# Kernel tuning notes

Hardware: AMD Instinct MI355X
Metric: run time of the kernel (lower is better)

Reference implementation:

```python
import jax, jax.numpy as jnp
import numpy as np

B = 16; DEMO = 5; COND = 50; QOI = 50
L = DEMO * (COND + 2 * QOI)  # 750
D = 1024; H = 16; HD = D // H; NL = 6; DFF = 4096
IN_DIM = 5; OUT_DIM = 2; MAXPOS = max(COND, QOI)
NEG = -1e9


def _build_consts():
    # token types per demo segment: 0=cond, 1=qoi_kv, 2=qoi_k (query)
    types, demo, pos = [], [], []
    for d in range(DEMO):
        types += [0] * COND + [1] * QOI + [2] * QOI
        demo += [d] * (COND + 2 * QOI)
        pos += list(range(COND)) + list(range(QOI)) + list(range(QOI))
    t = np.array(types); g = np.array(demo); p = np.array(pos)
    ti, tj = t[:, None], t[None, :]
    gi, gj = g[:, None], g[None, :]
    eye = np.arange(L)[:, None] == np.arange(L)[None, :]
    prev = (gj < gi) & (tj < 2)                      # attend to cond/qoi_kv of earlier demos
    same = (gj == gi) & ((tj == 0) | ((ti == 1) & (tj == 1)) | ((ti == 2) & eye))
    mask = prev | same                               # True = allowed
    out_idx = np.where(t == 2)[0]                    # qoi_k positions -> outputs
    return mask, p, out_idx


def setup_inputs():
    key = jax.random.key(0)
    ks = jax.random.split(key, 10)
    mask, pos, out_idx = _build_consts()
    s = 0.02
    return {
        'sequence': jax.random.normal(ks[0], (B, L, IN_DIM), jnp.float32),
        'pre_W': jax.random.normal(ks[1], (IN_DIM, D), jnp.float32) * s,
        'pre_b': jnp.zeros((D,), jnp.float32),
        'pe_table': jax.random.normal(ks[2], (MAXPOS, D), jnp.float32) * s,
        'Wqkv': jax.random.normal(ks[3], (NL, D, 3 * D), jnp.float32) * s,
        'bqkv': jnp.zeros((NL, 3 * D), jnp.float32),
        'Wo': jax.random.normal(ks[4], (NL, D, D), jnp.float32) * s,
        'bo': jnp.zeros((NL, D), jnp.float32),
        'ln1_g': jnp.ones((NL, D), jnp.float32), 'ln1_b': jnp.zeros((NL, D), jnp.float32),
        'ln2_g': jnp.ones((NL, D), jnp.float32), 'ln2_b': jnp.zeros((NL, D), jnp.float32),
        'W1': jax.random.normal(ks[5], (NL, D, DFF), jnp.float32) * s,
        'b1': jnp.zeros((NL, DFF), jnp.float32),
        'W2': jax.random.normal(ks[6], (NL, DFF, D), jnp.float32) * s,
        'b2': jnp.zeros((NL, D), jnp.float32),
        'post_W': jax.random.normal(ks[7], (D, OUT_DIM), jnp.float32) * s,
        'post_b': jnp.zeros((OUT_DIM,), jnp.float32),
        'basic_mask': jnp.asarray(mask),
        'index_pos': jnp.asarray(pos, jnp.int32),
        'out_idx': jnp.asarray(out_idx, jnp.int32),
    }


def _ln(x, g, b):
    m = jnp.mean(x, axis=-1, keepdims=True)
    v = jnp.var(x, axis=-1, keepdims=True)
    return (x - m) * jax.lax.rsqrt(v + 1e-5) * g + b


def _encoder(x, bias, Wqkv, bqkv, Wo, bo, ln1_g, ln1_b, ln2_g, ln2_b, W1, b1, W2, b2):
    scale = 1.0 / np.sqrt(HD)
    for l in range(NL):
        qkv = x @ Wqkv[l] + bqkv[l]                          # [B,L,3D]
        q, k, v = jnp.split(qkv, 3, axis=-1)
        hd = lambda t: t.reshape(B, L, H, HD).transpose(0, 2, 1, 3)
        q, k, v = hd(q), hd(k), hd(v)
        sc = jnp.einsum('bhqd,bhkd->bhqk', q, k) * scale + bias
        a = jax.nn.softmax(sc, axis=-1)
        o = jnp.einsum('bhqk,bhkd->bhqd', a, v).transpose(0, 2, 1, 3).reshape(B, L, D)
        x = _ln(x + o @ Wo[l] + bo[l], ln1_g[l], ln1_b[l])   # post-LN (torch default)
        h = jax.nn.gelu(x @ W1[l] + b1[l], approximate=False)
        x = _ln(x + h @ W2[l] + b2[l], ln2_g[l], ln2_b[l])
    return x


def reference(sequence, pre_W, pre_b, pe_table, Wqkv, bqkv, Wo, bo,
              ln1_g, ln1_b, ln2_g, ln2_b, W1, b1, W2, b2,
              post_W, post_b, basic_mask, index_pos, out_idx):
    x = sequence @ pre_W + pre_b + pe_table[index_pos]       # pre-projection + learned PE
    bias = jnp.where(basic_mask, 0.0, NEG)[None, None, :, :]  # ~basic_mask -> -inf additive
    x = _encoder(x, bias, Wqkv, bqkv, Wo, bo, ln1_g, ln1_b, ln2_g, ln2_b, W1, b1, W2, b2)
    y = x @ post_W + post_b                                  # [B,L,OUT_DIM]
    y = y[:, out_idx, :]                                     # select qoi_k outputs
    return y.reshape(B, DEMO, QOI, OUT_DIM)
```

## Files before the change

kernel.cpp:

```cpp
#include <hip/hip_runtime.h>


#define Bz  16
#define Lz  750
#define Dz  1024
#define Hz  16
#define HDz 64
#define NLz 6
#define DFFz 4096
#define Mz  (Bz*Lz)
#define VSTRIDE 768
#define QKVPART ((size_t)Bz*Hz*Lz*HDz)

typedef unsigned short u16;
typedef unsigned int   u32;
typedef unsigned long long u64;
typedef __attribute__((ext_vector_type(8))) short bf8;
typedef __attribute__((ext_vector_type(4))) float f4;
typedef __attribute__((ext_vector_type(4))) unsigned short u16x4;

__device__ __forceinline__ u16 f2b(float f){
  u32 u = __builtin_bit_cast(u32, f);
  u += 0x7fffu + ((u >> 16) & 1u);
  return (u16)(u >> 16);
}
__device__ __forceinline__ u32 cvtpk(float a, float b){
  u32 r;
  asm("v_cvt_pk_bf16_f32 %0, %1, %2" : "=v"(r) : "v"(a), "v"(b));
  return r;
}
__device__ __forceinline__ void glds16(const void* g, void* l){
  __builtin_amdgcn_global_load_lds((const __attribute__((address_space(1))) void*)g,
                                   (__attribute__((address_space(3))) void*)l, 16, 0, 0);
}

__global__ __launch_bounds__(256) void k_mask(u64* __restrict__ mb){
  const int idx = blockIdx.x*256 + threadIdx.x;
  if (idx >= Lz*12) return;
  const int q = idx / 12, kt = idx - q*12;
  const int gq = q/150, rq = q - gq*150;
  const int tq = rq < 50 ? 0 : (rq < 100 ? 1 : 2);
  u64 m = 0;
  for (int j = 0; j < 64; j++){
    const int k = kt*64 + j;
    if (k >= Lz) break;
    const int gk = k/150, rk = k - gk*150;
    const int tk = rk < 50 ? 0 : (rk < 100 ? 1 : 2);
    const bool prev = (gk < gq) && (tk < 2);
    const bool same = (gk == gq) && ((tk == 0) || (tq == 1 && tk == 1) || (tq == 2 && k == q));
    if (prev || same) m |= (1ull << j);
  }
  mb[idx] = m;
}

__global__ __launch_bounds__(256) void k_embed(const float* __restrict__ seq,
    const float* __restrict__ preW, const float* __restrict__ preb,
    const float* __restrict__ pe, float* __restrict__ x, u16* __restrict__ xb){
  const int m = blockIdx.x, t = threadIdx.x;
  const int l = m % Lz;
  const int r = l % 150;
  const int p = r < 50 ? r : (r < 100 ? r - 50 : r - 100);
  const float s0 = seq[m*5+0], s1 = seq[m*5+1], s2 = seq[m*5+2],
              s3 = seq[m*5+3], s4 = seq[m*5+4];
  const int d = t*4;
  f4 acc = *(const f4*)&preb[d];
  acc += *(const f4*)&pe[p*Dz + d];
  acc += s0 * *(const f4*)&preW[0*Dz + d];
  acc += s1 * *(const f4*)&preW[1*Dz + d];
  acc += s2 * *(const f4*)&preW[2*Dz + d];
  acc += s3 * *(const f4*)&preW[3*Dz + d];
  acc += s4 * *(const f4*)&preW[4*Dz + d];
  *(f4*)&x[(size_t)m*Dz + d] = acc;
  u16x4 hv = { f2b(acc.x), f2b(acc.y), f2b(acc.z), f2b(acc.w) };
  *(u16x4*)&xb[(size_t)m*Dz + d] = hv;
}

__global__ __launch_bounds__(256) void k_transpose(const float* __restrict__ W,
    u16* __restrict__ Wt, int K, int ldw){
  __shared__ float tile[32][33];
  const int tx = threadIdx.x, ty = threadIdx.y;
  const int n0 = blockIdx.x*32, k0 = blockIdx.y*32;
  #pragma unroll
  for (int i = 0; i < 4; i++){
    const int k = ty + i*8;
    tile[k][tx] = W[(size_t)(k0+k)*ldw + n0+tx];
  }
  __syncthreads();
  #pragma unroll
  for (int i = 0; i < 4; i++){
    const int n = ty + i*8;
    Wt[(size_t)(n0+n)*K + k0+tx] = f2b(tile[tx][n]);
  }
}

template<int EPI>
__global__ __launch_bounds__(256, 2) void k_gemm(
    const u16* __restrict__ A, const u16* __restrict__ Bt,
    int M, int N, int K, int lda, int ldc, int col0,
    const float* __restrict__ bias,
    float* __restrict__ xres, u16* __restrict__ outb, u16* __restrict__ vtb){
  __shared__ u16 As[128*64];
  __shared__ u16 Bs[128*64];
  const int t = threadIdx.x;
  const int m0 = blockIdx.x*128, n0 = blockIdx.y*128;
  const int w = t >> 6, lane = t & 63;
  const int wm = (w >> 1)*64, wn = (w & 1)*64;
  const int cl = lane & 15, g4 = lane >> 4;
  f4 acc[4][4] = {};
  const int srow = t >> 3, scol = (t & 7)*8;
  const int lds_off = srow*64 + scol;
  for (int k0 = 0; k0 < K; k0 += 64){
    #pragma unroll
    for (int c = 0; c < 4; c++){
      int ra = m0 + c*32 + srow; ra = ra < M ? ra : M-1;
      glds16(A + (size_t)ra*lda + k0 + scol, &As[c*2048 + lds_off]);
      const int rb = n0 + c*32 + srow;
      glds16(Bt + (size_t)rb*K + k0 + scol, &Bs[c*2048 + lds_off]);
    }
    __syncthreads();
    #pragma unroll
    for (int kk = 0; kk < 2; kk++){
      const int ko = kk*32 + g4*8;
      bf8 af[4], bfr[4];
      #pragma unroll
      for (int i = 0; i < 4; i++) af[i]  = *(const bf8*)&As[(wm + i*16 + cl)*64 + ko];
      #pragma unroll
      for (int j = 0; j < 4; j++) bfr[j] = *(const bf8*)&Bs[(wn + j*16 + cl)*64 + ko];
      #pragma unroll
      for (int i = 0; i < 4; i++)
        #pragma unroll
        for (int j = 0; j < 4; j++)
          acc[i][j] = __builtin_amdgcn_mfma_f32_16x16x32_bf16(af[i], bfr[j], acc[i][j], 0, 0, 0);
    }
    __syncthreads();
  }
  const int rl = g4*4;
  #pragma unroll
  for (int i = 0; i < 4; i++){
    #pragma unroll
    for (int j = 0; j < 4; j++){
      const int gn = n0 + wn + j*16 + cl;
      const float bsv = bias ? bias[gn] : 0.f;
      if constexpr (EPI == 0){
        const int part = gn >> 10;
        const int hh = (gn >> 6) & 15;
        const int dd = gn & 63;
        const int gm0 = m0 + wm + i*16 + rl;
        if (part == 2){
          if (gm0 + 3 < M){
            const int b = gm0 / Lz, lr0 = gm0 - b*Lz;
            const float v0 = acc[i][j][0] + bsv, v1 = acc[i][j][1] + bsv;
            const float v2 = acc[i][j][2] + bsv, v3 = acc[i][j][3] + bsv;
            if (lr0 <= Lz - 4){
              u32* dst = (u32*)&vtb[((size_t)(b*Hz + hh)*HDz + dd)*VSTRIDE + lr0];
              dst[0] = cvtpk(v0, v1);
              dst[1] = cvtpk(v2, v3);
            } else {
              #pragma unroll
              for (int r = 0; r < 4; r++){
                const int gm = gm0 + r;
                const int br = gm / Lz, lr = gm - br*Lz;
                vtb[((size_t)(br*Hz + hh)*HDz + dd)*VSTRIDE + lr] = f2b(acc[i][j][r] + bsv);
              }
            }
          }
        } else {
          #pragma unroll
          for (int r = 0; r < 4; r++){
            const int gm = gm0 + r;
            if (gm < M){
              const int b = gm / Lz, lr = gm - b*Lz;
              outb[(size_t)part*QKVPART + ((size_t)(b*Hz + hh)*Lz + lr)*HDz + dd]
                  = f2b(acc[i][j][r] + bsv);
            }
          }
        }
      } else {
        #pragma unroll
        for (int r = 0; r < 4; r++){
          const int gm = m0 + wm + i*16 + rl + r;
          if (gm < M){
            const float v = acc[i][j][r] + bsv;
            if constexpr (EPI == 1){
              xres[(size_t)gm*ldc + col0 + gn] += v;
            } else {
              const float ge = 0.5f*v*(1.0f + erff(v*0.70710678f));
              outb[(size_t)gm*ldc + col0 + gn] = f2b(ge);
            }
          }
        }
      }
    }
  }
}

__global__ __launch_bounds__(64, 3) void k_attn(const u16* __restrict__ qb,
    const u16* __restrict__ kb, const u16* __restrict__ vt,
    const u64* __restrict__ mb, u16* __restrict__ ob){
  __shared__ u32 Ps[1024];
  const int t = threadIdx.x;
  const int cl = t & 15, g4 = t >> 4;
  const int bh = blockIdx.y, b = bh >> 4, h = bh & 15;
  const int bx = blockIdx.x;
  const u16* qhp = qb + (size_t)bh*(Lz*HDz);
  const u16* khp = kb + (size_t)bh*(Lz*HDz);
  const u16* vhp = vt + (size_t)bh*(HDz*VSTRIDE);
  const float SC = 0.18033688011112042f;
  const f4 z4 = {0.f, 0.f, 0.f, 0.f};

  for (int half = 0; half < 2; half++){
    const int c = half ? (23 - bx) : bx;
    const int q0 = c*32;
    bf8 qfr[2][2];
    int qc[2];
    #pragma unroll
    for (int qf = 0; qf < 2; qf++){
      const int q = q0 + qf*16 + cl;
      qc[qf] = q < Lz ? q : Lz-1;
      #pragma unroll
      for (int kk = 0; kk < 2; kk++)
        qfr[qf][kk] = *(const bf8*)&qhp[(size_t)qc[qf]*HDz + kk*32 + g4*8];
    }
    int qmax = q0 + 31; if (qmax > Lz-1) qmax = Lz-1;
    const int gqm = qmax/150;
    int kmax = gqm*150 + 100; if (qmax + 1 > kmax) kmax = qmax + 1;
    const int nt = (kmax + 63) >> 6;

    f4 oacc[4][2] = {};
    float mrun[2] = {-1e30f, -1e30f}, lrun[2] = {0.f, 0.f};

    for (int kt = 0; kt < nt; kt++){
      const int kstart = kt*64;
      u32 mlo[2], mhi[2];
      #pragma unroll
      for (int qf = 0; qf < 2; qf++){
        const u64 m = mb[qc[qf]*12 + kt];
        mlo[qf] = (u32)m; mhi[qf] = (u32)(m >> 32);
      }
      f4 sacc[4][2];
      __builtin_amdgcn_s_setprio(1);
      #pragma unroll
      for (int kk = 0; kk < 2; kk++){
        bf8 kfr[4];
        #pragma unroll
        for (int kf = 0; kf < 4; kf++)
          kfr[kf] = *(const bf8*)&khp[(size_t)(kstart + kf*16 + cl)*HDz + kk*32 + g4*8];
        #pragma unroll
        for (int kf = 0; kf < 4; kf++)
          #pragma unroll
          for (int qf = 0; qf < 2; qf++)
            sacc[kf][qf] = __builtin_amdgcn_mfma_f32_16x16x32_bf16(kfr[kf], qfr[qf][kk],
                             kk == 0 ? z4 : sacc[kf][qf], 0, 0, 0);
      }
      __builtin_amdgcn_s_setprio(0);
      float own0 = -1e30f, own1 = -1e30f;
      #pragma unroll
      for (int kf = 0; kf < 4; kf++){
        #pragma unroll
        for (int rr = 0; rr < 4; rr++){
          const float s0 = sacc[kf][0][rr]*SC;
          const float s1 = sacc[kf][1][rr]*SC;
          sacc[kf][0][rr] = s0; sacc[kf][1][rr] = s1;
          own0 = fmaxf(own0, s0); own1 = fmaxf(own1, s1);
        }
      }
      own0 = fmaxf(own0, __shfl_xor(own0, 16)); own0 = fmaxf(own0, __shfl_xor(own0, 32));
      own1 = fmaxf(own1, __shfl_xor(own1, 16)); own1 = fmaxf(own1, __shfl_xor(own1, 32));
      const float mn0 = fmaxf(mrun[0], own0), mn1 = fmaxf(mrun[1], own1);
      const float sc0 = exp2f(mrun[0] - mn0), sc1 = exp2f(mrun[1] - mn1);
      float sum0 = 0.f, sum1 = 0.f;
      #pragma unroll
      for (int kf = 0; kf < 4; kf++){
        #pragma unroll
        for (int qf = 0; qf < 2; qf++){
          const float mn = qf ? mn1 : mn0;
          const u32 w16 = ((kf & 2) ? mhi[qf] : mlo[qf]) >> ((kf & 1)*16);
          const u32 wq = w16 >> (g4*4);
          f4 p;
          #pragma unroll
          for (int rr = 0; rr < 4; rr++){
            const float pe = exp2f(sacc[kf][qf][rr] - mn);
            p[rr] = ((wq >> rr) & 1u) ? pe : 0.f;
            if (qf == 0) sum0 += p[rr]; else sum1 += p[rr];
          }
          const u32 lo = cvtpk(p[0], p[1]);
          const u32 hi = cvtpk(p[2], p[3]);
          const int kk = kf >> 1;
          const int tg4 = ((kf & 1) << 1) | (g4 >> 1);
          const int widx = (qf*2 + kk)*256 + tg4*64 + cl*4 + (g4 & 1)*2;
          *(u64*)&Ps[widx] = ((u64)hi << 32) | lo;
        }
      }
      sum0 += __shfl_xor(sum0, 16); sum0 += __shfl_xor(sum0, 32);
      sum1 += __shfl_xor(sum1, 16); sum1 += __shfl_xor(sum1, 32);
      lrun[0] = lrun[0]*sc0 + sum0; mrun[0] = mn0;
      lrun[1] = lrun[1]*sc1 + sum1; mrun[1] = mn1;
      #pragma unroll
      for (int df = 0; df < 4; df++){
        oacc[df][0] *= sc0;
        oacc[df][1] *= sc1;
      }
      __builtin_amdgcn_s_setprio(1);
      #pragma unroll
      for (int kk = 0; kk < 2; kk++){
        bf8 vfr[4];
        #pragma unroll
        for (int df = 0; df < 4; df++)
          vfr[df] = *(const bf8*)&vhp[(size_t)(df*16 + cl)*VSTRIDE + kstart + kk*32 + g4*8];
        bf8 pw[2];
        #pragma unroll
        for (int qf = 0; qf < 2; qf++)
          pw[qf] = *(const bf8*)&Ps[(qf*2 + kk)*256 + g4*64 + cl*4];
        #pragma unroll
        for (int df = 0; df < 4; df++)
          #pragma unroll
          for (int qf = 0; qf < 2; qf++)
            oacc[df][qf] = __builtin_amdgcn_mfma_f32_16x16x32_bf16(vfr[df], pw[qf], oacc[df][qf], 0, 0, 0);
      }
      __builtin_amdgcn_s_setprio(0);
    }
    #pragma unroll
    for (int qf = 0; qf < 2; qf++){
      const int q = q0 + qf*16 + cl;
      if (q < Lz){
        const float inv = 1.f / lrun[qf];
        #pragma unroll
        for (int df = 0; df < 4; df++){
          u16x4 hv = { f2b(oacc[df][qf][0]*inv), f2b(oacc[df][qf][1]*inv),
                       f2b(oacc[df][qf][2]*inv), f2b(oacc[df][qf][3]*inv) };
          *(u16x4*)&ob[((size_t)b*Lz + q)*Dz + h*HDz + df*16 + g4*4] = hv;
        }
      }
    }
  }
}

__global__ __launch_bounds__(256) void k_ln(float* __restrict__ x, u16* __restrict__ xb,
    const float* __restrict__ g, const float* __restrict__ bb){
  const int m = blockIdx.x, t = threadIdx.x;
  float* xr = x + (size_t)m*Dz;
  f4 v = *(const f4*)&xr[t*4];
  float s = v.x + v.y + v.z + v.w;
  float q = v.x*v.x + v.y*v.y + v.z*v.z + v.w*v.w;
  #pragma unroll
  for (int off = 1; off < 64; off <<= 1){
    s += __shfl_xor(s, off);
    q += __shfl_xor(q, off);
  }
  __shared__ float ss[4], sq[4];
  const int w = t >> 6;
  if ((t & 63) == 0){ ss[w] = s; sq[w] = q; }
  __syncthreads();
  s = ss[0] + ss[1] + ss[2] + ss[3];
  q = sq[0] + sq[1] + sq[2] + sq[3];
  const float mean = s * (1.f/1024.f);
  const float var  = q * (1.f/1024.f) - mean*mean;
  const float rs = rsqrtf(var + 1e-5f);
  const f4 gg = *(const f4*)&g[t*4];
  const f4 bv = *(const f4*)&bb[t*4];
  f4 o;
  o.x = (v.x - mean)*rs*gg.x + bv.x;
  o.y = (v.y - mean)*rs*gg.y + bv.y;
  o.z = (v.z - mean)*rs*gg.z + bv.z;
  o.w = (v.w - mean)*rs*gg.w + bv.w;
  *(f4*)&xr[t*4] = o;
  u16x4 hv = { f2b(o.x), f2b(o.y), f2b(o.z), f2b(o.w) };
  *(u16x4*)&xb[(size_t)m*Dz + t*4] = hv;
}

__global__ __launch_bounds__(64) void k_out(const float* __restrict__ x,
    const float* __restrict__ pw, const float* __restrict__ pb, float* __restrict__ out){
  const int bid = blockIdx.x, lane = threadIdx.x;
  const int b = bid / 250, oi = bid - b*250;
  const int dd = oi / 50, qq = oi - dd*50;
  const int l = dd*150 + 100 + qq;
  const float* xr = x + ((size_t)b*Lz + l)*Dz;
  float a0 = 0.f, a1 = 0.f;
  #pragma unroll
  for (int c = 0; c < 4; c++){
    const int d = c*256 + lane*4;
    const f4 v  = *(const f4*)&xr[d];
    const f4 p0 = *(const f4*)&pw[2*d];
    const f4 p1 = *(const f4*)&pw[2*d + 4];
    a0 += v.x*p0.x + v.y*p0.z + v.z*p1.x + v.w*p1.z;
    a1 += v.x*p0.y + v.y*p0.w + v.z*p1.y + v.w*p1.w;
  }
  #pragma unroll
  for (int off = 32; off > 0; off >>= 1){
    a0 += __shfl_xor(a0, off);
    a1 += __shfl_xor(a1, off);
  }
  if (lane == 0){
    out[(size_t)bid*2 + 0] = a0 + pb[0];
    out[(size_t)bid*2 + 1] = a1 + pb[1];
  }
}

extern "C" void kernel_launch(void* const* d_in, const int* in_sizes, int n_in,
                              void* d_out, int out_size, void* d_ws, size_t ws_size,
                              hipStream_t stream){
  (void)in_sizes; (void)n_in; (void)out_size; (void)ws_size;
  const float* seq   = (const float*)d_in[0];
  const float* preW  = (const float*)d_in[1];
  const float* preb  = (const float*)d_in[2];
  const float* pe    = (const float*)d_in[3];
  const float* Wqkv  = (const float*)d_in[4];
  const float* bqkv  = (const float*)d_in[5];
  const float* Wo    = (const float*)d_in[6];
  const float* bo    = (const float*)d_in[7];
  const float* ln1g  = (const float*)d_in[8];
  const float* ln1b  = (const float*)d_in[9];
  const float* ln2g  = (const float*)d_in[10];
  const float* ln2b  = (const float*)d_in[11];
  const float* W1    = (const float*)d_in[12];
  const float* b1    = (const float*)d_in[13];
  const float* W2    = (const float*)d_in[14];
  const float* b2    = (const float*)d_in[15];
  const float* postW = (const float*)d_in[16];
  const float* postb = (const float*)d_in[17];
  float* out = (float*)d_out;

  char* ws = (char*)d_ws;
  float* x  = (float*)(ws + 0);
  u16*   xb = (u16*)(ws + 49152000);
  u16*   R  = (u16*)(ws + 73728000);
  u16* qB = R;
  u16* kB = R + QKVPART;
  u16* oB = R + 2*QKVPART;
  u16* vT = (u16*)(ws + 147456000);
  u16* wt = (u16*)(ws + 172621824);
  u64* mbp = (u64*)(ws + 178913280);
  u16* hB = R;

  k_mask<<<36, 256, 0, stream>>>(mbp);
  k_embed<<<Mz, 256, 0, stream>>>(seq, preW, preb, pe, x, xb);
  const dim3 tb(32, 8);
  for (int l = 0; l < NLz; l++){
    k_transpose<<<dim3(96, 32), tb, 0, stream>>>(Wqkv + (size_t)l*1024*3072, wt, 1024, 3072);
    k_gemm<0><<<dim3(94, 24), 256, 0, stream>>>(xb, wt, Mz, 3072, 1024, 1024, 0, 0,
                                                bqkv + l*3072, nullptr, qB, vT);
    k_attn<<<dim3(12, 256), 64, 0, stream>>>(qB, kB, vT, mbp, oB);
    k_transpose<<<dim3(32, 32), tb, 0, stream>>>(Wo + (size_t)l*1024*1024, wt, 1024, 1024);
    k_gemm<1><<<dim3(94, 8), 256, 0, stream>>>(oB, wt, Mz, 1024, 1024, 1024, 1024, 0,
                                               bo + l*1024, x, nullptr, nullptr);
    k_ln<<<Mz, 256, 0, stream>>>(x, xb, ln1g + l*1024, ln1b + l*1024);
    for (int off = 0; off < 4096; off += 2048){
      k_transpose<<<dim3(64, 32), tb, 0, stream>>>(W1 + (size_t)l*1024*4096 + off, wt, 1024, 4096);
      k_gemm<2><<<dim3(94, 16), 256, 0, stream>>>(xb, wt, Mz, 2048, 1024, 1024, 4096, off,
                                                  b1 + l*4096 + off, nullptr, hB, nullptr);
    }
    for (int koff = 0; koff < 4096; koff += 2048){
      k_transpose<<<dim3(32, 64), tb, 0, stream>>>(W2 + (size_t)l*4096*1024 + (size_t)koff*1024,
                                                   wt, 2048, 1024);
      k_gemm<1><<<dim3(94, 8), 256, 0, stream>>>(hB + koff, wt, Mz, 1024, 2048, 4096, 1024, 0,
                                                 koff == 0 ? (b2 + l*1024) : nullptr, x, nullptr, nullptr);
    }
    k_ln<<<Mz, 256, 0, stream>>>(x, xb, ln2g + l*1024, ln2b + l*1024);
  }
  k_out<<<4000, 64, 0, stream>>>(x, postW, postb, out);
}
```

Baseline: 4.302 ms.

## Swizzle GEMM LDS layout, raise occupancy, and prefetch K/V in attention

Measured after the change: 4.360 ms. No clear change (+1.4%).

```diff
diff --git a/kernel.cpp b/kernel.cpp
--- a/kernel.cpp
+++ b/kernel.cpp
@@ -94,7 +94,7 @@
 }
 
 template<int EPI>
-__global__ __launch_bounds__(256, 2) void k_gemm(
+__global__ __launch_bounds__(256, 4) void k_gemm(
     const u16* __restrict__ A, const u16* __restrict__ Bt,
     int M, int N, int K, int lda, int ldc, int col0,
     const float* __restrict__ bias,
@@ -107,8 +107,9 @@
   const int wm = (w >> 1)*64, wn = (w & 1)*64;
   const int cl = lane & 15, g4 = lane >> 4;
   f4 acc[4][4] = {};
-  const int srow = t >> 3, scol = (t & 7)*8;
-  const int lds_off = srow*64 + scol;
+  const int srow = t >> 3, sg = t & 7;
+  const int scol = (sg ^ (srow & 7)) * 8;
+  const int lds_off = srow*64 + sg*8;
   for (int k0 = 0; k0 < K; k0 += 64){
     #pragma unroll
     for (int c = 0; c < 4; c++){
@@ -120,7 +121,7 @@
     __syncthreads();
     #pragma unroll
     for (int kk = 0; kk < 2; kk++){
-      const int ko = kk*32 + g4*8;
+      const int ko = ((kk*4 + g4) ^ (cl & 7)) * 8;
       bf8 af[4], bfr[4];
       #pragma unroll
       for (int i = 0; i < 4; i++) af[i]  = *(const bf8*)&As[(wm + i*16 + cl)*64 + ko];
@@ -229,6 +230,13 @@
     f4 oacc[4][2] = {};
     float mrun[2] = {-1e30f, -1e30f}, lrun[2] = {0.f, 0.f};
 
+    bf8 kfr[2][4];
+    #pragma unroll
+    for (int kk = 0; kk < 2; kk++)
+      #pragma unroll
+      for (int kf = 0; kf < 4; kf++)
+        kfr[kk][kf] = *(const bf8*)&khp[(size_t)(kf*16 + cl)*HDz + kk*32 + g4*8];
+
     for (int kt = 0; kt < nt; kt++){
       const int kstart = kt*64;
       u32 mlo[2], mhi[2];
@@ -240,19 +248,27 @@
       f4 sacc[4][2];
       __builtin_amdgcn_s_setprio(1);
       #pragma unroll
-      for (int kk = 0; kk < 2; kk++){
-        bf8 kfr[4];
-        #pragma unroll
-        for (int kf = 0; kf < 4; kf++)
-          kfr[kf] = *(const bf8*)&khp[(size_t)(kstart + kf*16 + cl)*HDz + kk*32 + g4*8];
+      for (int kk = 0; kk < 2; kk++)
         #pragma unroll
         for (int kf = 0; kf < 4; kf++)
           #pragma unroll
           for (int qf = 0; qf < 2; qf++)
-            sacc[kf][qf] = __builtin_amdgcn_mfma_f32_16x16x32_bf16(kfr[kf], qfr[qf][kk],
+            sacc[kf][qf] = __builtin_amdgcn_mfma_f32_16x16x32_bf16(kfr[kk][kf], qfr[qf][kk],
                              kk == 0 ? z4 : sacc[kf][qf], 0, 0, 0);
-      }
       __builtin_amdgcn_s_setprio(0);
+      bf8 vfr[2][4];
+      #pragma unroll
+      for (int kk = 0; kk < 2; kk++)
+        #pragma unroll
+        for (int df = 0; df < 4; df++)
+          vfr[kk][df] = *(const bf8*)&vhp[(size_t)(df*16 + cl)*VSTRIDE + kstart + kk*32 + g4*8];
+      if (kt + 1 < nt){
+        #pragma unroll
+        for (int kk = 0; kk < 2; kk++)
+          #pragma unroll
+          for (int kf = 0; kf < 4; kf++)
+            kfr[kk][kf] = *(const bf8*)&khp[(size_t)(kstart + 64 + kf*16 + cl)*HDz + kk*32 + g4*8];
+      }
       float own0 = -1e30f, own1 = -1e30f;
       #pragma unroll
       for (int kf = 0; kf < 4; kf++){
@@ -303,10 +319,6 @@
       __builtin_amdgcn_s_setprio(1);
       #pragma unroll
       for (int kk = 0; kk < 2; kk++){
-        bf8 vfr[4];
-        #pragma unroll
-        for (int df = 0; df < 4; df++)
-          vfr[df] = *(const bf8*)&vhp[(size_t)(df*16 + cl)*VSTRIDE + kstart + kk*32 + g4*8];
         bf8 pw[2];
         #pragma unroll
         for (int qf = 0; qf < 2; qf++)
@@ -315,7 +327,7 @@
         for (int df = 0; df < 4; df++)
           #pragma unroll
           for (int qf = 0; qf < 2; qf++)
-            oacc[df][qf] = __builtin_amdgcn_mfma_f32_16x16x32_bf16(vfr[df], pw[qf], oacc[df][qf], 0, 0, 0);
+            oacc[df][qf] = __builtin_amdgcn_mfma_f32_16x16x32_bf16(vfr[kk][df], pw[qf], oacc[df][qf], 0, 0, 0);
       }
       __builtin_amdgcn_s_setprio(0);
     }
```
